# Kernel optimization log

Measured on AMD Instinct MI355X. Metric: run time of the kernel, lower is better.

The kernel has to match this reference:

```python
import jax, jax.numpy as jnp
import numpy as np

N_HEAD = 8
N_EMBD = 768
T_MAX = 1024


def setup_inputs() -> dict:
    key = jax.random.key(0)
    ks = jax.random.split(key, 5)
    B, T, C = 8, 1024, N_EMBD
    x = jax.random.normal(ks[0], (B, T, C), dtype=jnp.float32)
    c_attn_weight = jax.random.normal(ks[1], (3 * C, C), dtype=jnp.float32) * (1.0 / np.sqrt(C))
    c_attn_bias = jax.random.normal(ks[2], (3 * C,), dtype=jnp.float32) * 0.02
    c_proj_weight = jax.random.normal(ks[3], (C, C), dtype=jnp.float32) * (1.0 / np.sqrt(C))
    c_proj_bias = jax.random.normal(ks[4], (C,), dtype=jnp.float32) * 0.02
    bias = jnp.tril(jnp.ones((T_MAX, T_MAX), dtype=jnp.int32))[None, None]  # (1,1,Tmax,Tmax)
    return {
        "x": x,
        "c_attn_weight": c_attn_weight,
        "c_attn_bias": c_attn_bias,
        "c_proj_weight": c_proj_weight,
        "c_proj_bias": c_proj_bias,
        "bias": bias,
    }


def reference(x, c_attn_weight, c_attn_bias, c_proj_weight, c_proj_bias, bias):
    B, T, C = x.shape
    H = N_HEAD
    D = C // H  # head dim
    qkv = jnp.einsum("btc,fc->btf", x, c_attn_weight) + c_attn_bias  # (B,T,3C)
    q, k, v = jnp.split(qkv, 3, axis=-1)
    q = q.reshape(B, T, H, D).transpose(0, 2, 1, 3)  # (B,H,T,D)
    k = k.reshape(B, T, H, D).transpose(0, 2, 1, 3)
    v = v.reshape(B, T, H, D).transpose(0, 2, 1, 3)
    att = jnp.einsum("bhqd,bhkd->bhqk", q, k) * (1.0 / np.sqrt(D))  # (B,H,T,T)
    mask = bias[:, :, :T, :T] == 0
    att = jnp.where(mask, jnp.float32(-jnp.inf), att)
    att = jax.nn.softmax(att, axis=-1)
    y = jnp.einsum("bhqk,bhkd->bhqd", att, v)  # (B,H,T,D)
    y = y.transpose(0, 2, 1, 3).reshape(B, T, C)
    y = jnp.einsum("btc,fc->btf", y, c_proj_weight) + c_proj_bias
    return y
```

## Files before the change

### kernel.cpp

```cpp
#include <hip/hip_runtime.h>
#include <hip/hip_bf16.h>
#include <stdint.h>


typedef unsigned short ushort_t;
typedef __attribute__((ext_vector_type(8))) short short8;
typedef __attribute__((ext_vector_type(4))) float floatx4;
typedef __attribute__((ext_vector_type(4))) unsigned short ushort4v;

#define MFMA16(a, b, c) __builtin_amdgcn_mfma_f32_16x16x32_bf16(a, b, c, 0, 0, 0)
#define NEG_BIG (-1e30f)

__device__ __forceinline__ unsigned short f2bf(float f) {
  union { float f; unsigned int u; } v; v.f = f;
  unsigned int r = (v.u + 0x7FFFu + ((v.u >> 16) & 1u)) >> 16;
  return (unsigned short)r;
}

__device__ __forceinline__ unsigned int packbf2(float a, float b) {
  union { __hip_bfloat162 h; unsigned int u; } cv;
  cv.h = __float22bfloat162_rn(make_float2(a, b));
  return cv.u;
}

#define GLOAD16(src, dst)                                              \
  __builtin_amdgcn_global_load_lds(                                    \
      (const __attribute__((address_space(1))) void*)(src),            \
      (__attribute__((address_space(3))) void*)(dst), 16, 0, 0)

#define WAITBAR(VM)                                                    \
  do {                                                                 \
    asm volatile("s_waitcnt vmcnt(" #VM ")" ::: "memory");             \
    __builtin_amdgcn_s_barrier();                                      \
  } while (0)

#define WAITBAR_LGKM(VM)                                               \
  do {                                                                 \
    asm volatile("s_waitcnt vmcnt(" #VM ") lgkmcnt(0)" ::: "memory");  \
    __builtin_amdgcn_s_barrier();                                      \
  } while (0)

__global__ __launch_bounds__(256) void cvt3(
    const float* __restrict__ x, const float* __restrict__ wa,
    const float* __restrict__ wp, ushort_t* __restrict__ xb,
    ushort_t* __restrict__ wab, ushort_t* __restrict__ wpb)
{
  const int n1 = (8192 * 768) / 4, n2 = (2304 * 768) / 4;
  int i = blockIdx.x * 256 + threadIdx.x;
  const float* in; ushort_t* out;
  if (i < n1)            { in = x;  out = xb; }
  else if (i < n1 + n2)  { in = wa; out = wab; i -= n1; }
  else                   { in = wp; out = wpb; i -= (n1 + n2); }
  float4 v = *(const float4*)(in + (size_t)i * 4);
  ushort4v o;
  o.x = f2bf(v.x); o.y = f2bf(v.y); o.z = f2bf(v.z); o.w = f2bf(v.w);
  *(ushort4v*)(out + (size_t)i * 4) = o;
}

#define GSTAGE(LA, LB, OFF)                                            \
  do {                                                                 \
    GLOAD16(gA + (OFF), &LA[wid * 512]);                               \
    GLOAD16(gA + (OFF) + (size_t)64 * 768, &LA[wid * 512 + 64 * 32]);  \
    GLOAD16(gB + (OFF), &LB[wid * 512]);                               \
    GLOAD16(gB + (OFF) + (size_t)64 * 768, &LB[wid * 512 + 64 * 32]);  \
  } while (0)

#define GSTEP(LA, LB, OFF, STG, VM)                                    \
  do {                                                                 \
    asm volatile("s_waitcnt vmcnt(" #VM ")" ::: "memory");             \
    __builtin_amdgcn_s_barrier();                                      \
    short8 af[4], bf[4];                                               \
    _Pragma("unroll")                                                  \
    for (int t_ = 0; t_ < 4; ++t_) {                                   \
      af[t_] = *(const short8*)&LA[(wm + t_ * 16 + l15) * 32 + sw];    \
      bf[t_] = *(const short8*)&LB[(wn + t_ * 16 + l15) * 32 + sw];    \
    }                                                                  \
    asm volatile("s_waitcnt lgkmcnt(0)" ::: "memory");                 \
    __builtin_amdgcn_s_barrier();                                      \
    if (STG) GSTAGE(LA, LB, OFF);                                      \
    __builtin_amdgcn_s_setprio(1);                                     \
    _Pragma("unroll")                                                  \
    for (int tm = 0; tm < 4; ++tm)                                     \
      _Pragma("unroll")                                                \
      for (int tn = 0; tn < 4; ++tn)                                   \
        acc[tm][tn] = MFMA16(af[tm], bf[tn], acc[tm][tn]);             \
    __builtin_amdgcn_s_setprio(0);                                     \
  } while (0)

#define GK2(T)                                                         \
  GSTEP(As0, Bs0, ((T) + 2) * 32, 1, 4);                               \
  GSTEP(As1, Bs1, ((T) + 3) * 32, 1, 4);

#define GEMM_KLOOP                                                     \
  GSTAGE(As0, Bs0, 0); GSTAGE(As1, Bs1, 32);                           \
  GK2(0) GK2(2) GK2(4) GK2(6) GK2(8) GK2(10)                           \
  GK2(12) GK2(14) GK2(16) GK2(18) GK2(20)                              \
  GSTEP(As0, Bs0, 0, 0, 4);                                            \
  GSTEP(As1, Bs1, 0, 0, 0);

#define GEMM_DECLS                                                     \
  __shared__ ushort_t As0[128 * 32], As1[128 * 32];                    \
  __shared__ ushort_t Bs0[128 * 32], Bs1[128 * 32];                    \
  const int tid  = threadIdx.x;                                        \
  const int lane = tid & 63;                                           \
  const int l15  = lane & 15;                                          \
  const int quad = lane >> 4;                                          \
  const int wid  = tid >> 6;                                           \
  const int m0 = blockIdx.x * 128;                                     \
  const int n0 = blockIdx.y * 128;                                     \
  const int wm = (wid >> 1) * 64;                                      \
  const int wn = (wid & 1) * 64;                                       \
  const int srow = tid >> 2;                                           \
  const int scol = (((tid & 3) ^ ((srow ^ (srow >> 2)) & 3))) * 8;     \
  const int sw = (quad ^ ((l15 ^ (l15 >> 2)) & 3)) * 8;                \
  floatx4 acc[4][4] = {};

__global__ __launch_bounds__(256) void gemm_qkv(
    const ushort_t* __restrict__ A,
    const ushort_t* __restrict__ W,
    const float* __restrict__ bias,
    ushort_t* __restrict__ QK,
    ushort_t* __restrict__ VT)
{
  GEMM_DECLS;

  const ushort_t* gA = A + (size_t)(m0 + srow) * 768 + scol;
  const ushort_t* gB = W + (size_t)(n0 + srow) * 768 + scol;

  GEMM_KLOOP;

  const float QSCALE = 0.10206207261596577f * 1.4426950408889634f;

#pragma unroll
  for (int tn = 0; tn < 4; ++tn) {
    const int gc = n0 + wn + tn * 16 + l15;
    const float bv = bias[gc];
    const bool isv = (gc >= 1536);
    const bool isq = (gc < 768);
    const int hh = (gc - 1536) / 96, dd = (gc - 1536) % 96;
#pragma unroll
    for (int tm = 0; tm < 4; ++tm) {
      const int gr = m0 + wm + tm * 16 + quad * 4;
#pragma unroll
      for (int r = 0; r < 4; ++r) {
        float val = acc[tm][tn][r] + bv;
        const int row = gr + r;
        if (!isv) {
          if (isq) val *= QSCALE;
          QK[(size_t)row * 1536 + gc] = f2bf(val);
        } else {
          const int bb = row >> 10, tt = row & 1023;
          const int tt2 = (tt & ~0x1C) | (((tt >> 4) & 1) << 2) |
                          (((tt >> 2) & 3) << 3);
          VT[(((size_t)(bb * 8 + hh)) * 96 + dd) * 1024 + tt2] = f2bf(val);
        }
      }
    }
  }
}

__global__ __launch_bounds__(256) void gemm_proj(
    const ushort_t* __restrict__ A,
    const ushort_t* __restrict__ W,
    const float* __restrict__ bias,
    float* __restrict__ C,
    int M, int N)
{
  GEMM_DECLS;

  const ushort_t* gA = A + (size_t)(m0 + srow) * 768 + scol;
  const ushort_t* gB = W + (size_t)(n0 + srow) * 768 + scol;

  GEMM_KLOOP;

#pragma unroll
  for (int tn = 0; tn < 4; ++tn) {
    const int gc = n0 + wn + tn * 16 + l15;
    const float bv = bias[gc];
#pragma unroll
    for (int tm = 0; tm < 4; ++tm) {
      const int gr = m0 + wm + tm * 16 + quad * 4;
#pragma unroll
      for (int r = 0; r < 4; ++r)
        C[(size_t)(gr + r) * N + gc] = acc[tm][tn][r] + bv;
    }
  }
}

#define ATTN_COMPUTE(KS, VTC, K0)                                      \
  do {                                                                 \
    floatx4 s[4] = {};                                                 \
    __builtin_amdgcn_s_setprio(1);                                     \
    _Pragma("unroll")                                                  \
    for (int t = 0; t < 4; ++t) {                                      \
      _Pragma("unroll")                                                \
      for (int c = 0; c < 3; ++c) {                                    \
        short8 kf = *(const short8*)                                   \
            &KS[(t * 16 + l15) * 96 + c * 32 + quad * 8];              \
        s[t] = MFMA16(kf, qf[c], s[t]);                                \
      }                                                                \
    }                                                                  \
    __builtin_amdgcn_s_setprio(0);                                     \
    float p[4][4];                                                     \
    if ((K0) + 64 <= q0w) {                                            \
      _Pragma("unroll")                                                \
      for (int t = 0; t < 4; ++t)                                      \
        _Pragma("unroll")                                              \
        for (int j = 0; j < 4; ++j) p[t][j] = s[t][j];                 \
    } else {                                                           \
      const int kq = (K0) + quad * 4;                                  \
      _Pragma("unroll")                                                \
      for (int t = 0; t < 4; ++t)                                      \
        _Pragma("unroll")                                              \
        for (int j = 0; j < 4; ++j)                                    \
          p[t][j] = (kq + t * 16 + j <= rq) ? s[t][j] : NEG_BIG;       \
    }                                                                  \
    float m0v = fmaxf(fmaxf(p[0][0], p[0][1]), fmaxf(p[0][2], p[0][3]));\
    float m1v = fmaxf(fmaxf(p[1][0], p[1][1]), fmaxf(p[1][2], p[1][3]));\
    float m2v = fmaxf(fmaxf(p[2][0], p[2][1]), fmaxf(p[2][2], p[2][3]));\
    float m3v = fmaxf(fmaxf(p[3][0], p[3][1]), fmaxf(p[3][2], p[3][3]));\
    float mt = fmaxf(fmaxf(m0v, m1v), fmaxf(m2v, m3v));                \
    mt = fmaxf(mt, __shfl_xor(mt, 16));                                \
    mt = fmaxf(mt, __shfl_xor(mt, 32));                                \
    if (!__all(mt - m_i <= 8.0f)) {                                    \
      const float mn = fmaxf(m_i, mt);                                 \
      const float al = __builtin_amdgcn_exp2f(m_i - mn);               \
      m_i = mn;                                                        \
      l_i *= al;                                                       \
      _Pragma("unroll")                                                \
      for (int j = 0; j < 4; ++j) {                                    \
        const float alr = __shfl(al, quad * 4 + j);                    \
        _Pragma("unroll")                                              \
        for (int f = 0; f < 6; ++f) O[f][j] *= alr;                    \
      }                                                                \
    }                                                                  \
    float rs = 0.f;                                                    \
    _Pragma("unroll")                                                  \
    for (int t = 0; t < 4; ++t)                                        \
      _Pragma("unroll")                                                \
      for (int j = 0; j < 4; ++j) {                                    \
        p[t][j] = __builtin_amdgcn_exp2f(p[t][j] - m_i);               \
        rs += p[t][j];                                                 \
      }                                                                \
    rs += __shfl_xor(rs, 16);                                          \
    rs += __shfl_xor(rs, 32);                                          \
    l_i += rs;                                                         \
    union { short8 s8; unsigned int u[4]; } pf0, pf1;                  \
    pf0.u[0] = packbf2(p[0][0], p[0][1]);                              \
    pf0.u[1] = packbf2(p[0][2], p[0][3]);                              \
    pf0.u[2] = packbf2(p[1][0], p[1][1]);                              \
    pf0.u[3] = packbf2(p[1][2], p[1][3]);                              \
    pf1.u[0] = packbf2(p[2][0], p[2][1]);                              \
    pf1.u[1] = packbf2(p[2][2], p[2][3]);                              \
    pf1.u[2] = packbf2(p[3][0], p[3][1]);                              \
    pf1.u[3] = packbf2(p[3][2], p[3][3]);                              \
    __builtin_amdgcn_s_setprio(1);                                     \
    _Pragma("unroll")                                                  \
    for (int f = 0; f < 6; ++f) {                                      \
      short8 vf0 = *(const short8*)&VTC[(f * 16 + l15) * 72 + quad * 8];\
      O[f] = MFMA16(pf0.s8, vf0, O[f]);                                \
      short8 vf1 = *(const short8*)                                    \
          &VTC[(f * 16 + l15) * 72 + 32 + quad * 8];                   \
      O[f] = MFMA16(pf1.s8, vf1, O[f]);                                \
    }                                                                  \
    __builtin_amdgcn_s_setprio(0);                                     \
  } while (0)

#define AITER(KS, VTC, KSN, VTN, K0)                                   \
  do {                                                                 \
    const int k0_ = (K0);                                              \
    const int nk_ = k0_ + 64;                                          \
    WAITBAR_LGKM(3);                                                   \
    _Pragma("unroll")                                                  \
    for (int i = 0; i < 3; ++i) {                                      \
      const int e = ke0 + i * 512;                                     \
      const int kr = e / 96, kc = e % 96;                              \
      GLOAD16(QK + (rowbase + nk_ + kr) * 1536 + 768 + qoff + kc,      \
              &KSN[wid * 1536 + i * 512]);                             \
    }                                                                  \
    ATTN_COMPUTE(KS, VTC, k0_);                                        \
    _Pragma("unroll")                                                  \
    for (int g = 0; g < 3; ++g)                                        \
      *(short8*)&VTN[(g * 32 + vd) * 72 + vkc] = vreg[g];              \
    if (nk_ + 64 < kend) {                                             \
      _Pragma("unroll")                                                \
      for (int g = 0; g < 3; ++g)                                      \
        vreg[g] = *(const short8*)                                     \
            (vtb + (size_t)(g * 32 + vd) * 1024 + nk_ + 64 + vkc);     \
    }                                                                  \
  } while (0)

#define AITER_LAST(KS, VTC, K0)                                        \
  do {                                                                 \
    WAITBAR_LGKM(0);                                                   \
    ATTN_COMPUTE(KS, VTC, (K0));                                       \
  } while (0)

__global__ __launch_bounds__(256) void attn_fused(
    const ushort_t* __restrict__ QK,
    const ushort_t* __restrict__ VT,
    ushort_t* __restrict__ y)
{
  __shared__ ushort_t Ks0[64 * 96], Ks1[64 * 96];
  __shared__ ushort_t Vt0[96 * 72], Vt1[96 * 72];

  const int tid  = threadIdx.x;
  const int lane = tid & 63;
  const int l15  = lane & 15;
  const int quad = lane >> 4;
  const int wid  = tid >> 6;

  const int lin = blockIdx.x + (blockIdx.y << 4);
  const int swz = ((lin & 7) << 7) + (lin >> 3);
  const int chunk = swz & 15;
  const int bh = swz >> 4;
  const int b = bh >> 3;
  const int h = bh & 7;
  const int qoff = h * 96;

  const int q0w = chunk * 64 + wid * 16;
  const int kend = chunk * 64 + 64;
  const int rq = q0w + l15;

  const size_t rowbase = (size_t)b * 1024;
  const ushort_t* vtb = VT + (size_t)bh * 96 * 1024;

  const int ke0 = wid * 1536 + lane * 8;
  const int vd  = (tid >> 3);
  const int vkc = (tid & 7) * 8;

  short8 qf[3];
#pragma unroll
  for (int c = 0; c < 3; ++c)
    qf[c] = *(const short8*)(QK + (rowbase + q0w + l15) * 1536 + qoff +
                             c * 32 + quad * 8);

  float m_i = NEG_BIG;
  float l_i = 0.f;
  floatx4 O[6] = {};

  short8 vreg[3];

#pragma unroll
  for (int g = 0; g < 3; ++g)
    vreg[g] = *(const short8*)(vtb + (size_t)(g * 32 + vd) * 1024 + vkc);
#pragma unroll
  for (int i = 0; i < 3; ++i) {
    const int e = ke0 + i * 512;
    const int kr = e / 96, kc = e % 96;
    GLOAD16(QK + (rowbase + kr) * 1536 + 768 + qoff + kc,
            &Ks0[wid * 1536 + i * 512]);
  }
#pragma unroll
  for (int g = 0; g < 3; ++g)
    *(short8*)&Vt0[(g * 32 + vd) * 72 + vkc] = vreg[g];
#pragma unroll
  for (int g = 0; g < 3; ++g)
    vreg[g] = *(const short8*)(vtb + (size_t)(g * 32 + vd) * 1024 + 64 + vkc);

  int k0 = 0;
  while (k0 + 128 < kend) {
    AITER(Ks0, Vt0, Ks1, Vt1, k0);
    AITER(Ks1, Vt1, Ks0, Vt0, k0 + 64);
    k0 += 128;
  }
  if (k0 + 64 < kend) {
    AITER(Ks0, Vt0, Ks1, Vt1, k0);
    AITER_LAST(Ks1, Vt1, k0 + 64);
  } else {
    AITER_LAST(Ks0, Vt0, k0);
  }

  float inv[4];
#pragma unroll
  for (int j = 0; j < 4; ++j) {
    const float lj = __shfl(l_i, quad * 4 + j);
    inv[j] = 1.0f / fmaxf(lj, 1e-20f);
  }
#pragma unroll
  for (int j = 0; j < 4; ++j) {
    const size_t row = rowbase + q0w + quad * 4 + j;
#pragma unroll
    for (int f = 0; f < 6; ++f)
      y[row * 768 + qoff + f * 16 + l15] = f2bf(O[f][j] * inv[j]);
  }
}

extern "C" void kernel_launch(void* const* d_in, const int* in_sizes, int n_in,
                              void* d_out, int out_size, void* d_ws, size_t ws_size,
                              hipStream_t stream)
{
  const float* x_f  = (const float*)d_in[0];
  const float* wa_f = (const float*)d_in[1];
  const float* ba_f = (const float*)d_in[2];
  const float* wp_f = (const float*)d_in[3];
  const float* bp_f = (const float*)d_in[4];
  float* out = (float*)d_out;

  ushort_t* xb  = (ushort_t*)d_ws;
  ushort_t* wab = xb  + (size_t)8192 * 768;
  ushort_t* wpb = wab + (size_t)2304 * 768;
  ushort_t* QK  = wpb + (size_t)768 * 768;
  ushort_t* VT  = QK  + (size_t)8192 * 1536;
  ushort_t* yw  = VT  + (size_t)8192 * 768;

  cvt3<<<8448, 256, 0, stream>>>(x_f, wa_f, wp_f, xb, wab, wpb);

  gemm_qkv<<<dim3(64, 18), 256, 0, stream>>>(xb, wab, ba_f, QK, VT);
  attn_fused<<<dim3(16, 64), 256, 0, stream>>>(QK, VT, yw);
  gemm_proj<<<dim3(64, 6), 256, 0, stream>>>(yw, wpb, bp_f, out,
                                             8192, 768);
}
```

Measured before the change: 204.7 us.

## Rewrite QKV GEMM with 256x256 tiles, 8 waves and phased pipelining

The QKV projection GEMM moves from 128x128 tiles with 4 waves and K=32 steps to 256x256 tiles with 8 waves and K=64 double-buffered LDS stages. Global loads are interleaved across eight compute phases, and a grid swizzle remaps block indices for cache locality. The aim is more operand reuse per LDS load and fewer barriers per FLOP. In exchange it uses 128KB of LDS, a larger accumulator footprint, and only 288 blocks, which may leave some CUs idle.

```diff
diff --git a/kernel.cpp b/kernel.cpp
--- a/kernel.cpp
+++ b/kernel.cpp
@@ -57,93 +57,127 @@
   *(ushort4v*)(out + (size_t)i * 4) = o;
 }
 
-#define GSTAGE(LA, LB, OFF)                                            \
-  do {                                                                 \
-    GLOAD16(gA + (OFF), &LA[wid * 512]);                               \
-    GLOAD16(gA + (OFF) + (size_t)64 * 768, &LA[wid * 512 + 64 * 32]);  \
-    GLOAD16(gB + (OFF), &LB[wid * 512]);                               \
-    GLOAD16(gB + (OFF) + (size_t)64 * 768, &LB[wid * 512 + 64 * 32]);  \
-  } while (0)
-
-#define GSTEP(LA, LB, OFF, STG, VM)                                    \
-  do {                                                                 \
-    asm volatile("s_waitcnt vmcnt(" #VM ")" ::: "memory");             \
+#define STG_A(BUF, PART, T)                                            \
+  do {                                                                 \
+    const int r0_ = (PART) * 64 + arow0;                               \
+    GLOAD16(Ag + (size_t)(m0 + r0_) * 768 + (T) * 64 + esrc,           \
+            &Ab[BUF][r0_ * 64 + ecol]);                                \
+    GLOAD16(Ag + (size_t)(m0 + r0_ + 128) * 768 + (T) * 64 + esrc,     \
+            &Ab[BUF][(r0_ + 128) * 64 + ecol]);                        \
+  } while (0)
+
+#define STG_B(BUF, PART, T)                                            \
+  do {                                                                 \
+    const int r0_ = (PART) * 32 + brow0;                               \
+    GLOAD16(Bg + (size_t)(n0 + r0_) * 768 + (T) * 64 + esrc,           \
+            &Bb[BUF][r0_ * 64 + ecol]);                                \
+    GLOAD16(Bg + (size_t)(n0 + r0_ + 128) * 768 + (T) * 64 + esrc,     \
+            &Bb[BUF][(r0_ + 128) * 64 + ecol]);                        \
+  } while (0)
+
+#define PHASE(BUF, MH, NH, STAGE_CODE, WAIT_CODE)                      \
+  do {                                                                 \
+    short8 af_[4][2], bf_[2][2];                                       \
+    _Pragma("unroll")                                                  \
+    for (int i_ = 0; i_ < 4; ++i_)                                     \
+      _Pragma("unroll")                                                \
+      for (int k_ = 0; k_ < 2; ++k_)                                   \
+        af_[i_][k_] = *(const short8*)&Ab[BUF][                        \
+            (wm2 * 128 + ((MH) * 4 + i_) * 16 + l15) * 64 +            \
+            ((k_ * 32 + quad * 8) ^ swzr)];                            \
+    _Pragma("unroll")                                                  \
+    for (int n_ = 0; n_ < 2; ++n_)                                     \
+      _Pragma("unroll")                                                \
+      for (int k_ = 0; k_ < 2; ++k_)                                   \
+        bf_[n_][k_] = *(const short8*)&Bb[BUF][                        \
+            (wn4 * 64 + ((NH) * 2 + n_) * 16 + l15) * 64 +             \
+            ((k_ * 32 + quad * 8) ^ swzr)];                            \
+    STAGE_CODE;                                                        \
+    asm volatile("" ::: "memory");                                     \
     __builtin_amdgcn_s_barrier();                                      \
-    short8 af[4], bf[4];                                               \
-    _Pragma("unroll")                                                  \
-    for (int t_ = 0; t_ < 4; ++t_) {                                   \
-      af[t_] = *(const short8*)&LA[(wm + t_ * 16 + l15) * 32 + sw];    \
-      bf[t_] = *(const short8*)&LB[(wn + t_ * 16 + l15) * 32 + sw];    \
-    }                                                                  \
-    asm volatile("s_waitcnt lgkmcnt(0)" ::: "memory");                 \
+    __builtin_amdgcn_s_setprio(1);                                     \
+    _Pragma("unroll")                                                  \
+    for (int i_ = 0; i_ < 4; ++i_)                                     \
+      _Pragma("unroll")                                                \
+      for (int n_ = 0; n_ < 2; ++n_)                                   \
+        _Pragma("unroll")                                              \
+        for (int k_ = 0; k_ < 2; ++k_)                                 \
+          acc[(MH) * 4 + i_][(NH) * 2 + n_] =                          \
+              MFMA16(af_[i_][k_], bf_[n_][k_],                         \
+                     acc[(MH) * 4 + i_][(NH) * 2 + n_]);               \
+    __builtin_amdgcn_s_setprio(0);                                     \
+    WAIT_CODE;                                                         \
+    asm volatile("" ::: "memory");                                     \
     __builtin_amdgcn_s_barrier();                                      \
-    if (STG) GSTAGE(LA, LB, OFF);                                      \
-    __builtin_amdgcn_s_setprio(1);                                     \
-    _Pragma("unroll")                                                  \
-    for (int tm = 0; tm < 4; ++tm)                                     \
-      _Pragma("unroll")                                                \
-      for (int tn = 0; tn < 4; ++tn)                                   \
-        acc[tm][tn] = MFMA16(af[tm], bf[tn], acc[tm][tn]);             \
-    __builtin_amdgcn_s_setprio(0);                                     \
-  } while (0)
-
-#define GK2(T)                                                         \
-  GSTEP(As0, Bs0, ((T) + 2) * 32, 1, 4);                               \
-  GSTEP(As1, Bs1, ((T) + 3) * 32, 1, 4);
-
-#define GEMM_KLOOP                                                     \
-  GSTAGE(As0, Bs0, 0); GSTAGE(As1, Bs1, 32);                           \
-  GK2(0) GK2(2) GK2(4) GK2(6) GK2(8) GK2(10)                           \
-  GK2(12) GK2(14) GK2(16) GK2(18) GK2(20)                              \
-  GSTEP(As0, Bs0, 0, 0, 4);                                            \
-  GSTEP(As1, Bs1, 0, 0, 0);
-
-#define GEMM_DECLS                                                     \
-  __shared__ ushort_t As0[128 * 32], As1[128 * 32];                    \
-  __shared__ ushort_t Bs0[128 * 32], Bs1[128 * 32];                    \
-  const int tid  = threadIdx.x;                                        \
-  const int lane = tid & 63;                                           \
-  const int l15  = lane & 15;                                          \
-  const int quad = lane >> 4;                                          \
-  const int wid  = tid >> 6;                                           \
-  const int m0 = blockIdx.x * 128;                                     \
-  const int n0 = blockIdx.y * 128;                                     \
-  const int wm = (wid >> 1) * 64;                                      \
-  const int wn = (wid & 1) * 64;                                       \
-  const int srow = tid >> 2;                                           \
-  const int scol = (((tid & 3) ^ ((srow ^ (srow >> 2)) & 3))) * 8;     \
-  const int sw = (quad ^ ((l15 ^ (l15 >> 2)) & 3)) * 8;                \
-  floatx4 acc[4][4] = {};
-
-__global__ __launch_bounds__(256) void gemm_qkv(
-    const ushort_t* __restrict__ A,
-    const ushort_t* __restrict__ W,
+  } while (0)
+
+__global__ __launch_bounds__(512) void gemm_qkv(
+    const ushort_t* __restrict__ Ag,
+    const ushort_t* __restrict__ Bg,
     const float* __restrict__ bias,
     ushort_t* __restrict__ QK,
     ushort_t* __restrict__ VT)
 {
-  GEMM_DECLS;
-
-  const ushort_t* gA = A + (size_t)(m0 + srow) * 768 + scol;
-  const ushort_t* gB = W + (size_t)(n0 + srow) * 768 + scol;
-
-  GEMM_KLOOP;
+  __shared__ ushort_t Ab[2][256 * 64];
+  __shared__ ushort_t Bb[2][256 * 64];
+
+  const int tid  = threadIdx.x;
+  const int lane = tid & 63;
+  const int l15  = lane & 15;
+  const int quad = lane >> 4;
+  const int wid  = tid >> 6;
+  const int wm2  = wid >> 2;
+  const int wn4  = wid & 3;
+
+  const int lin = blockIdx.x + blockIdx.y * 32;
+  const int swz = (lin & 7) * 36 + (lin >> 3);
+  const int m0 = (swz & 31) * 256;
+  const int n0 = (swz >> 5) * 256;
+
+  const int arow0 = tid >> 3;
+  const int brow0 = ((tid >> 3) & 31) + (((tid >> 3) >> 5) << 6);
+  const int ecol  = (tid & 7) << 3;
+  const int esrc  = ecol ^ (((tid >> 5) & 1) << 4);
+  const int swzr  = ((l15 >> 2) & 1) << 4;
+
+  floatx4 acc[8][4] = {};
+
+  STG_A(0, 0, 0); STG_A(0, 1, 0); STG_B(0, 0, 0); STG_B(0, 1, 0);
+  STG_A(1, 0, 1); STG_B(1, 0, 1);
+  WAITBAR(4);
+
+#pragma unroll
+  for (int j = 0; j < 6; ++j) {
+    const int t1 = 2 * j + 1, t2 = 2 * j + 2, t3 = 2 * j + 3;
+    const bool s2 = (j < 5);
+    PHASE(0, 0, 0, { STG_A(1, 1, t1); STG_B(1, 1, t1); }, );
+    PHASE(0, 0, 1, , );
+    PHASE(0, 1, 0, { if (s2) STG_A(0, 0, t2); }, );
+    PHASE(0, 1, 1, { if (s2) STG_B(0, 0, t2); },
+          { if (s2) asm volatile("s_waitcnt vmcnt(4)" ::: "memory");
+            else    asm volatile("s_waitcnt vmcnt(0)" ::: "memory"); });
+    PHASE(1, 0, 0, { if (s2) STG_A(0, 1, t2); }, );
+    PHASE(1, 0, 1, { if (s2) STG_B(0, 1, t2); }, );
+    PHASE(1, 1, 0, { if (s2) STG_A(1, 0, t3); }, );
+    PHASE(1, 1, 1, { if (s2) STG_B(1, 0, t3); },
+          { if (s2) asm volatile("s_waitcnt vmcnt(4)" ::: "memory"); });
+  }
 
   const float QSCALE = 0.10206207261596577f * 1.4426950408889634f;
 
 #pragma unroll
-  for (int tn = 0; tn < 4; ++tn) {
-    const int gc = n0 + wn + tn * 16 + l15;
+  for (int fn = 0; fn < 4; ++fn) {
+    const int gc = n0 + wn4 * 64 + fn * 16 + l15;
     const float bv = bias[gc];
     const bool isv = (gc >= 1536);
     const bool isq = (gc < 768);
     const int hh = (gc - 1536) / 96, dd = (gc - 1536) % 96;
 #pragma unroll
-    for (int tm = 0; tm < 4; ++tm) {
-      const int gr = m0 + wm + tm * 16 + quad * 4;
+    for (int fm = 0; fm < 8; ++fm) {
+      const int gr = m0 + wm2 * 128 + fm * 16 + quad * 4;
 #pragma unroll
       for (int r = 0; r < 4; ++r) {
-        float val = acc[tm][tn][r] + bv;
+        float val = acc[fm][fn][r] + bv;
         const int row = gr + r;
         if (!isv) {
           if (isq) val *= QSCALE;
@@ -159,6 +193,47 @@
   }
 }
 
+#define GSTAGE(LA, LB, OFF)                                            \
+  do {                                                                 \
+    GLOAD16(gA + (OFF), &LA[wid * 512]);                               \
+    GLOAD16(gA + (OFF) + (size_t)64 * 768, &LA[wid * 512 + 64 * 32]);  \
+    GLOAD16(gB + (OFF), &LB[wid * 512]);                               \
+    GLOAD16(gB + (OFF) + (size_t)64 * 768, &LB[wid * 512 + 64 * 32]);  \
+  } while (0)
+
+#define GSTEP(LA, LB, OFF, STG, VM)                                    \
+  do {                                                                 \
+    asm volatile("s_waitcnt vmcnt(" #VM ")" ::: "memory");             \
+    __builtin_amdgcn_s_barrier();                                      \
+    short8 af[4], bf[4];                                               \
+    _Pragma("unroll")                                                  \
+    for (int t_ = 0; t_ < 4; ++t_) {                                   \
+      af[t_] = *(const short8*)&LA[(wm + t_ * 16 + l15) * 32 + sw];    \
+      bf[t_] = *(const short8*)&LB[(wn + t_ * 16 + l15) * 32 + sw];    \
+    }                                                                  \
+    asm volatile("s_waitcnt lgkmcnt(0)" ::: "memory");                 \
+    __builtin_amdgcn_s_barrier();                                      \
+    if (STG) GSTAGE(LA, LB, OFF);                                      \
+    __builtin_amdgcn_s_setprio(1);                                     \
+    _Pragma("unroll")                                                  \
+    for (int tm = 0; tm < 4; ++tm)                                     \
+      _Pragma("unroll")                                                \
+      for (int tn = 0; tn < 4; ++tn)                                   \
+        acc[tm][tn] = MFMA16(af[tm], bf[tn], acc[tm][tn]);             \
+    __builtin_amdgcn_s_setprio(0);                                     \
+  } while (0)
+
+#define GK2(T)                                                         \
+  GSTEP(As0, Bs0, ((T) + 2) * 32, 1, 4);                               \
+  GSTEP(As1, Bs1, ((T) + 3) * 32, 1, 4);
+
+#define GEMM_KLOOP                                                     \
+  GSTAGE(As0, Bs0, 0); GSTAGE(As1, Bs1, 32);                           \
+  GK2(0) GK2(2) GK2(4) GK2(6) GK2(8) GK2(10)                           \
+  GK2(12) GK2(14) GK2(16) GK2(18) GK2(20)                              \
+  GSTEP(As0, Bs0, 0, 0, 4);                                            \
+  GSTEP(As1, Bs1, 0, 0, 0);
+
 __global__ __launch_bounds__(256) void gemm_proj(
     const ushort_t* __restrict__ A,
     const ushort_t* __restrict__ W,
@@ -166,7 +241,21 @@
     float* __restrict__ C,
     int M, int N)
 {
-  GEMM_DECLS;
+  __shared__ ushort_t As0[128 * 32], As1[128 * 32];
+  __shared__ ushort_t Bs0[128 * 32], Bs1[128 * 32];
+  const int tid  = threadIdx.x;
+  const int lane = tid & 63;
+  const int l15  = lane & 15;
+  const int quad = lane >> 4;
+  const int wid  = tid >> 6;
+  const int m0 = blockIdx.x * 128;
+  const int n0 = blockIdx.y * 128;
+  const int wm = (wid >> 1) * 64;
+  const int wn = (wid & 1) * 64;
+  const int srow = tid >> 2;
+  const int scol = (((tid & 3) ^ ((srow ^ (srow >> 2)) & 3))) * 8;
+  const int sw = (quad ^ ((l15 ^ (l15 >> 2)) & 3)) * 8;
+  floatx4 acc[4][4] = {};
 
   const ushort_t* gA = A + (size_t)(m0 + srow) * 768 + scol;
   const ushort_t* gB = W + (size_t)(n0 + srow) * 768 + scol;
@@ -274,7 +363,7 @@
     _Pragma("unroll")                                                  \
     for (int i = 0; i < 3; ++i) {                                      \
       const int e = ke0 + i * 512;                                     \
-      const int kr = e / 96, kc = e % 96;                              \
+      const int kr = e / 96, kc = e % 96;                               \
       GLOAD16(QK + (rowbase + nk_ + kr) * 1536 + 768 + qoff + kc,      \
               &KSN[wid * 1536 + i * 512]);                             \
     }                                                                  \
@@ -406,7 +495,7 @@
 
   cvt3<<<8448, 256, 0, stream>>>(x_f, wa_f, wp_f, xb, wab, wpb);
 
-  gemm_qkv<<<dim3(64, 18), 256, 0, stream>>>(xb, wab, ba_f, QK, VT);
+  gemm_qkv<<<dim3(32, 9), 512, 0, stream>>>(xb, wab, ba_f, QK, VT);
   attn_fused<<<dim3(16, 64), 256, 0, stream>>>(QK, VT, yw);
   gemm_proj<<<dim3(64, 6), 256, 0, stream>>>(yw, wpb, bp_f, out,
                                              8192, 768);
```

Result: slower. 274.9 us (+34.3%).
